# Optimization experiments

Measured on AMD Instinct MI355X. Metric: run time of the kernel, lower is better.

Reference implementation:

```python
import jax, jax.numpy as jnp
from jax import lax
import numpy as np

T = 8   # num_samples
D = 7   # num_nodes
K = 3   # topk


def _normalize(v):
    return v / jnp.maximum(jnp.linalg.norm(v, axis=-1, keepdims=True), 1e-12)


def _pool(x):
    # AdaptiveMaxPool2d(1): [B,H,N,C,h,w] -> [B,H,N,C]
    return x.max(axis=(-2, -1))


def _sepconv(x, dw, dwb, pw, pwb):
    # depthwise 3x3 (pad 1) + pointwise 1x1, NCHW
    c = x.shape[1]
    y = lax.conv_general_dilated(x, dw, (1, 1), ((1, 1), (1, 1)),
                                 dimension_numbers=('NCHW', 'OIHW', 'NCHW'),
                                 feature_group_count=c)
    y = y + dwb[None, :, None, None]
    y = lax.conv_general_dilated(y, pw, (1, 1), 'VALID',
                                 dimension_numbers=('NCHW', 'OIHW', 'NCHW'))
    return y + pwb[None, :, None, None]


def _conv_iter(x, A, dw, dwb, pw, pwb):
    # x: [B,H,N,C,h,w], A: [B,H,M,N] -> aggregate then sepconv update
    x = jnp.einsum('bhnm,bhmcij->bhncij', A, x)
    B, H, N, C, h, w = x.shape
    y = x.transpose(0, 2, 1, 3, 4, 5).reshape(B * N, H * C, h, w)
    y = _sepconv(y, dw, dwb, pw, pwb)
    return y.reshape(B, N, H, C, h, w).transpose(0, 2, 1, 3, 4, 5)


def reference(x, alpha_if, alpha_tm1, alpha_rev, alpha_tm2,
              bias_if, bias_tm1, bias_rev, bias_tm2,
              if_dw, if_dwb, if_pw, if_pwb,
              tm1_dw, tm1_dwb, tm1_pw, tm1_pwb,
              rev_dw, rev_dwb, rev_pw, rev_pwb,
              tm2_dw, tm2_dwb, tm2_pw, tm2_pwb,
              tr_dw, tr_dwb, tr_pw, tr_pwb):
    B, H, Nall, C, hh, ww = x.shape
    normal = x[:, :, 1:]            # [B,H,T*D,C,h,w]
    master = x[:, :, 0:1]           # [B,H,1,C,h,w]
    # 'b h (t d) c i j -> (b t) h d c i j'
    normal = normal.reshape(B, H, T, D, C, hh, ww).transpose(0, 2, 1, 3, 4, 5, 6).reshape(B * T, H, D, C, hh, ww)

    # inter-frame adjacency
    vn = _normalize(_pool(normal))
    A = jax.nn.softmax(jnp.einsum('bhnc,bhmc->bhnm', vn, vn) / alpha_if + bias_if, axis=-1)
    normal = _conv_iter(normal, A, if_dw, if_dwb, if_pw, if_pwb)

    # to master 1
    temp = normal.reshape(B, T, H, D, C, hh, ww).transpose(0, 2, 1, 3, 4, 5, 6).reshape(B, H, T * D, C, hh, ww)
    all_node = jnp.concatenate([master, temp], axis=2)   # [B,H,57,...]
    vn = _normalize(_pool(all_node))
    A = jax.nn.softmax(jnp.einsum('bhnc,bhmc->bhnm', vn[:, :, 0:1], vn) / alpha_tm1 + bias_tm1, axis=-1)
    master = _conv_iter(all_node, A, tm1_dw, tm1_dwb, tm1_pw, tm1_pwb)  # [B,H,1,C,h,w]

    # transform normal nodes
    Bt = B * T
    y = normal.transpose(0, 2, 1, 3, 4, 5).reshape(Bt * D, H * C, hh, ww)
    y = _sepconv(y, tr_dw, tr_dwb, tr_pw, tr_pwb)
    normal = y.reshape(Bt, D, H, C, hh, ww).transpose(0, 2, 1, 3, 4, 5)

    # reverse: topk MOST-DISSIMILAR frames (largest=False on similarity)
    temp = normal.reshape(B, T, H, D, C, hh, ww).transpose(0, 2, 1, 3, 4, 5, 6)  # [B,H,T,D,C,h,w]
    main = temp[:, :, :, -1]                                 # [B,H,T,C,h,w]
    mv = _normalize(_pool(main))                              # [B,H,T,C]
    Asim = jnp.einsum('bhtc,bhsc->bhts', mv, mv)
    idx = lax.top_k(-Asim, K)[1]                              # [B,H,T,K] smallest-sim frames
    bi = jnp.arange(B)[:, None, None, None]
    hi = jnp.arange(H)[None, :, None, None]
    sel = temp[bi, hi, idx]                                   # [B,H,T,K,D,C,h,w]
    different = sel.transpose(0, 2, 1, 3, 4, 5, 6, 7).reshape(Bt, H, K * D, C, hh, ww)

    vd = _normalize(_pool(different))
    vo = _normalize(_pool(normal))
    A = jax.nn.softmax(-jnp.einsum('bhnc,bhmc->bhnm', vo, vd) / alpha_rev + bias_rev, axis=-1)
    normal = _conv_iter(different, A, rev_dw, rev_dwb, rev_pw, rev_pwb) + normal

    # to master 2
    temp = normal.reshape(B, T, H, D, C, hh, ww).transpose(0, 2, 1, 3, 4, 5, 6).reshape(B, H, T * D, C, hh, ww)
    all_node = jnp.concatenate([master, temp], axis=2)
    vn = _normalize(_pool(all_node))
    A = jax.nn.softmax(jnp.einsum('bhnc,bhmc->bhnm', vn[:, :, 0:1], vn) / alpha_tm2 + bias_tm2, axis=-1)
    master = _conv_iter(all_node, A, tm2_dw, tm2_dwb, tm2_pw, tm2_pwb)
    return master[:, :, 0]                                    # [B,H,C,h,w]


def setup_inputs() -> dict:
    key = jax.random.key(0)
    ks = jax.random.split(key, 16)
    B, H, C, hh, ww = 4, 4, 128, 14, 14
    DIM = 512
    w_scale = 0.05

    def sep(k):
        k1, k2 = jax.random.split(k)
        return (jax.random.normal(k1, (DIM, 1, 3, 3), jnp.float32) * w_scale,
                jnp.zeros((DIM,), jnp.float32),
                jax.random.normal(k2, (DIM, DIM, 1, 1), jnp.float32) * w_scale,
                jnp.zeros((DIM,), jnp.float32))

    if_dw, if_dwb, if_pw, if_pwb = sep(ks[1])
    tm1_dw, tm1_dwb, tm1_pw, tm1_pwb = sep(ks[2])
    rev_dw, rev_dwb, rev_pw, rev_pwb = sep(ks[3])
    tm2_dw, tm2_dwb, tm2_pw, tm2_pwb = sep(ks[4])
    tr_dw, tr_dwb, tr_pw, tr_pwb = sep(ks[5])

    return dict(
        x=jax.random.normal(ks[0], (B, H, 1 + T * D, C, hh, ww), jnp.float32),
        alpha_if=jnp.ones((), jnp.float32), alpha_tm1=jnp.ones((), jnp.float32),
        alpha_rev=jnp.ones((), jnp.float32), alpha_tm2=jnp.ones((), jnp.float32),
        bias_if=jnp.zeros((D, D), jnp.float32),
        bias_tm1=jnp.zeros((1, 1 + T * D), jnp.float32),
        bias_rev=jnp.zeros((D, K * D), jnp.float32),
        bias_tm2=jnp.zeros((1, 1 + T * D), jnp.float32),
        if_dw=if_dw, if_dwb=if_dwb, if_pw=if_pw, if_pwb=if_pwb,
        tm1_dw=tm1_dw, tm1_dwb=tm1_dwb, tm1_pw=tm1_pw, tm1_pwb=tm1_pwb,
        rev_dw=rev_dw, rev_dwb=rev_dwb, rev_pw=rev_pw, rev_pwb=rev_pwb,
        tm2_dw=tm2_dw, tm2_dwb=tm2_dwb, tm2_pw=tm2_pw, tm2_pwb=tm2_pwb,
        tr_dw=tr_dw, tr_dwb=tr_dwb, tr_pw=tr_pw, tr_pwb=tr_pwb,
    )
```

## Files before the change

### kernel.cpp

```cpp
#include <hip/hip_runtime.h>
#include <hip/hip_bf16.h>
#include <float.h>
#include <math.h>

#define B_    4
#define H_    4
#define T_    8
#define D_    7
#define C_    128
#define HH_   14
#define S_    196
#define S4_   49
#define BT_   32
#define HC_   512
#define NODE_ 57
#define K_    3
#define KD_   21

#define BIG_  (BT_*D_*HC_*S_)
#define MS_   (B_*HC_*S_)
#define UB_   (BT_*D_*S_)
#define UM_   (B_*S_)
#define UMP_  896
#define NT_   24
#define WS_   1024

typedef unsigned short u16;
typedef unsigned int   u32;
typedef short bf16x8 __attribute__((ext_vector_type(8)));
typedef float f32x4  __attribute__((ext_vector_type(4)));

__device__ __forceinline__ float wave_max(float v){
    #pragma unroll
    for(int o=32;o>0;o>>=1) v = fmaxf(v, __shfl_xor(v,o,64));
    return v;
}
__device__ __forceinline__ float wave_sum(float v){
    #pragma unroll
    for(int o=32;o>0;o>>=1) v += __shfl_xor(v,o,64);
    return v;
}
__device__ __forceinline__ u16 f2bf(float f){
    u32 u = __float_as_uint(f);
    u += 0x7FFF + ((u>>16)&1);
    return (u16)(u>>16);
}
__device__ __forceinline__ float bf2f(u16 h){ return __uint_as_float(((u32)h)<<16); }

__device__ __forceinline__ void gld16(const void* g, void* l){
    __builtin_amdgcn_global_load_lds(
        (__attribute__((address_space(1))) void*)(void*)g,
        (__attribute__((address_space(3))) void*)l, 16, 0, 0);
}

__global__ void k_pool_x(const float* __restrict__ x, float* __restrict__ out){
    int v = blockIdx.x*4 + (threadIdx.x>>6);
    int lane = threadIdx.x & 63;
    int c = v & (C_-1);
    int r = v >> 7;
    int d = r % D_; r /= D_;
    int h = r & (H_-1); r >>= 2;
    int bt = r;
    int b = bt >> 3, t = bt & 7;
    const float* row = x + ((size_t)((b*H_+h)*NODE_ + 1 + t*D_ + d)*C_ + c)*S_;
    float m = -FLT_MAX;
    for(int s=lane; s<S_; s+=64) m = fmaxf(m, row[s]);
    m = wave_max(m);
    if(lane==0) out[v] = m;
}

__global__ void k_pool_conv(const float* __restrict__ in, float* __restrict__ out){
    int v = blockIdx.x*4 + (threadIdx.x>>6);
    int lane = threadIdx.x & 63;
    int c = v & (C_-1);
    int r = v >> 7;
    int d = r % D_; r /= D_;
    int h = r & (H_-1); r >>= 2;
    int bt = r;
    const float* row = in + ((size_t)((bt*D_+d)*HC_ + h*C_ + c))*S_;
    float m = -FLT_MAX;
    for(int s=lane; s<S_; s+=64) m = fmaxf(m, row[s]);
    m = wave_max(m);
    if(lane==0) out[v] = m;
}

__global__ void k_pool_x_master(const float* __restrict__ x, float* __restrict__ out){
    int v = blockIdx.x*4 + (threadIdx.x>>6);
    int lane = threadIdx.x & 63;
    int c = v & (C_-1);
    int h = (v>>7) & (H_-1);
    int b = v >> 9;
    const float* row = x + ((size_t)((b*H_+h)*NODE_)*C_ + c)*S_;
    float m = -FLT_MAX;
    for(int s=lane; s<S_; s+=64) m = fmaxf(m, row[s]);
    m = wave_max(m);
    if(lane==0) out[v] = m;
}

__global__ void k_pool_m1(const float* __restrict__ in, float* __restrict__ out){
    int v = blockIdx.x*4 + (threadIdx.x>>6);
    int lane = threadIdx.x & 63;
    int c = v & (C_-1);
    int h = (v>>7) & (H_-1);
    int b = v >> 9;
    const float* row = in + ((size_t)(b*HC_ + h*C_ + c))*S_;
    float m = -FLT_MAX;
    for(int s=lane; s<S_; s+=64) m = fmaxf(m, row[s]);
    m = wave_max(m);
    if(lane==0) out[v] = m;
}

__global__ void k_normalize(float* __restrict__ v){
    int vec = blockIdx.x;
    float val = v[(size_t)vec*C_ + threadIdx.x];
    float ss = wave_sum(val*val);
    __shared__ float sh[2];
    if((threadIdx.x&63)==0) sh[threadIdx.x>>6] = ss;
    __syncthreads();
    float tot = sh[0]+sh[1];
    v[(size_t)vec*C_ + threadIdx.x] = val / fmaxf(sqrtf(tot), 1e-12f);
}

__global__ void k_A_if(const float* __restrict__ vn, const float* __restrict__ bias,
                       const float* __restrict__ alpha_p, float* __restrict__ A){
    int bh = blockIdx.x;
    __shared__ float vs[D_*C_];
    __shared__ float z[D_][D_];
    for(int e=threadIdx.x; e<D_*C_; e+=64) vs[e] = vn[(size_t)bh*D_*C_ + e];
    __syncthreads();
    float alpha = alpha_p[0];
    if(threadIdx.x < D_*D_){
        int n = threadIdx.x/D_, m = threadIdx.x%D_;
        float acc=0.f;
        for(int c=0;c<C_;c++) acc += vs[n*C_+c]*vs[m*C_+c];
        z[n][m] = acc/alpha + bias[n*D_+m];
    }
    __syncthreads();
    if(threadIdx.x < D_){
        int n = threadIdx.x;
        float mx=-FLT_MAX;
        for(int m=0;m<D_;m++) mx=fmaxf(mx,z[n][m]);
        float e[D_]; float sum=0.f;
        for(int m=0;m<D_;m++){ e[m]=expf(z[n][m]-mx); sum+=e[m]; }
        for(int m=0;m<D_;m++) A[((size_t)bh*D_+n)*D_+m] = e[m]/sum;
    }
}

__global__ void k_A_tm(const float* __restrict__ vm, const float* __restrict__ vnrm,
                       const float* __restrict__ bias, const float* __restrict__ alpha_p,
                       float* __restrict__ A){
    int bh = blockIdx.x;
    int b = bh>>2, h = bh&3;
    __shared__ float v0[C_];
    __shared__ float z[NODE_];
    for(int e=threadIdx.x;e<C_;e+=64) v0[e]=vm[(size_t)bh*C_+e];
    __syncthreads();
    float alpha=alpha_p[0];
    if(threadIdx.x<NODE_){
        int m=threadIdx.x;
        float acc=0.f;
        if(m==0){
            for(int c=0;c<C_;c++) acc+=v0[c]*v0[c];
        } else {
            int t=(m-1)/D_, d=(m-1)%D_;
            const float* vp = vnrm + (size_t)(((b*T_+t)*H_+h)*D_+d)*C_;
            for(int c=0;c<C_;c++) acc+=v0[c]*vp[c];
        }
        z[m]=acc/alpha + bias[m];
    }
    __syncthreads();
    if(threadIdx.x==0){
        float mx=-FLT_MAX;
        for(int m=0;m<NODE_;m++) mx=fmaxf(mx,z[m]);
        float sum=0.f;
        for(int m=0;m<NODE_;m++){ z[m]=expf(z[m]-mx); sum+=z[m]; }
        for(int m=0;m<NODE_;m++) A[(size_t)bh*NODE_+m]=z[m]/sum;
    }
}

__global__ void k_topk(const float* __restrict__ voHat, int* __restrict__ idx){
    int bh = blockIdx.x;
    int b = bh>>2, h = bh&3;
    __shared__ float mv[T_][C_];
    __shared__ float As[T_][T_];
    for(int e=threadIdx.x;e<T_*C_;e+=64){
        int t=e>>7, c=e&(C_-1);
        mv[t][c]=voHat[(size_t)(((b*T_+t)*H_+h)*D_+(D_-1))*C_+c];
    }
    __syncthreads();
    {
        int t=threadIdx.x>>3, s2=threadIdx.x&7;
        float acc=0.f;
        for(int c=0;c<C_;c++) acc+=mv[t][c]*mv[s2][c];
        As[t][s2]=acc;
    }
    __syncthreads();
    if(threadIdx.x<T_){
        int t=threadIdx.x;
        bool used[T_];
        for(int j=0;j<T_;j++) used[j]=false;
        for(int k=0;k<K_;k++){
            float mn=FLT_MAX; int bi=0;
            for(int s2=0;s2<T_;s2++){
                if(!used[s2] && As[t][s2]<mn){ mn=As[t][s2]; bi=s2; }
            }
            used[bi]=true;
            idx[((size_t)bh*T_+t)*K_+k]=bi;
        }
    }
}

__global__ void k_A_rev(const float* __restrict__ voHat, const int* __restrict__ idx,
                        const float* __restrict__ bias, const float* __restrict__ alpha_p,
                        float* __restrict__ A){
    int bth = blockIdx.x;
    int bt = bth>>2, h = bth&3;
    int b = bt>>3, t = bt&7;
    __shared__ float vo[D_][C_];
    __shared__ float vd[KD_][C_];
    __shared__ float z[D_][KD_];
    for(int e=threadIdx.x;e<D_*C_;e+=256){
        int n=e>>7, c=e&(C_-1);
        vo[n][c]=voHat[(size_t)((bt*H_+h)*D_+n)*C_+c];
    }
    for(int e=threadIdx.x;e<KD_*C_;e+=256){
        int m=e>>7, c=e&(C_-1);
        int k=m/D_, dp=m%D_;
        int tt=idx[((size_t)(b*H_+h)*T_+t)*K_+k];
        vd[m][c]=voHat[(size_t)(((b*T_+tt)*H_+h)*D_+dp)*C_+c];
    }
    __syncthreads();
    float alpha=alpha_p[0];
    if(threadIdx.x<D_*KD_){
        int n=threadIdx.x/KD_, m=threadIdx.x%KD_;
        float acc=0.f;
        for(int c=0;c<C_;c++) acc+=vo[n][c]*vd[m][c];
        z[n][m] = -acc/alpha + bias[n*KD_+m];
    }
    __syncthreads();
    if(threadIdx.x<D_){
        int n=threadIdx.x;
        float mx=-FLT_MAX;
        for(int m=0;m<KD_;m++) mx=fmaxf(mx,z[n][m]);
        float sum=0.f;
        for(int m=0;m<KD_;m++){ z[n][m]=expf(z[n][m]-mx); sum+=z[n][m]; }
        for(int m=0;m<KD_;m++) A[(size_t)((bt*H_+h)*D_+n)*KD_+m]=z[n][m]/sum;
    }
}

__global__ void k_agg_tm(const float* __restrict__ mastersrc, int master_is_x,
                         const float* __restrict__ normal, const float* __restrict__ A,
                         float* __restrict__ out){
    int v = blockIdx.x*256 + threadIdx.x;
    int s4 = v % S4_;
    int r  = v / S4_;
    int hc = r & (HC_-1);
    int b  = r >> 9;
    int h = hc >> 7, c = hc & (C_-1);
    const float* Ap = A + (size_t)(b*H_+h)*NODE_;
    f32x4 m0;
    if(master_is_x) m0 = *(const f32x4*)(mastersrc + ((size_t)((b*H_+h)*NODE_)*C_ + c)*S_ + s4*4);
    else            m0 = *(const f32x4*)(mastersrc + (size_t)(b*HC_+hc)*S_ + s4*4);
    f32x4 acc = Ap[0]*m0;
    for(int t=0;t<T_;t++){
        const float* np = normal + ((size_t)((b*T_+t)*D_)*HC_+hc)*S_ + s4*4;
        #pragma unroll
        for(int d=0;d<D_;d++)
            acc += Ap[1+t*D_+d] * *(const f32x4*)(np + (size_t)d*HC_*S_);
    }
    *(f32x4*)(out + (size_t)r*S_ + s4*4) = acc;
}

__device__ __forceinline__ void dw_split_tail(float (*ti)[S_], float (*to)[S_],
                                              const float* __restrict__ w,
                                              const float* __restrict__ bias,
                                              int img, int ch0,
                                              u16* __restrict__ Xh, u16* __restrict__ Xl){
    int tid = threadIdx.x;
    for(int e=tid; e<16*S_; e+=256){
        int chl = e/S_, s = e - (e/S_)*S_;
        int ch = ch0 + chl;
        int y = s/HH_, xx = s - (s/HH_)*HH_;
        float acc = bias[ch];
        #pragma unroll
        for(int ky=0;ky<3;ky++){
            int yy=y+ky-1;
            if(yy<0||yy>=HH_) continue;
            #pragma unroll
            for(int kx=0;kx<3;kx++){
                int xx2=xx+kx-1;
                if(xx2<0||xx2>=HH_) continue;
                acc += ti[chl][yy*HH_+xx2]*w[ch*9+ky*3+kx];
            }
        }
        to[chl][s]=acc;
    }
    __syncthreads();
    for(int e=tid; e<16*S_; e+=256){
        int s = e>>4, chl = e&15;
        float f = to[chl][s];
        u16 h = f2bf(f);
        float lo = f - bf2f(h);
        size_t o = ((size_t)img*S_ + s)*HC_ + ch0 + chl;
        Xh[o] = h;
        Xl[o] = f2bf(lo);
    }
}

__launch_bounds__(256)
__global__ void k_dwsplit(const float* __restrict__ in, const float* __restrict__ w,
                          const float* __restrict__ bias,
                          u16* __restrict__ Xh, u16* __restrict__ Xl){
    int img = blockIdx.x >> 5;
    int ch0 = (blockIdx.x & 31) * 16;
    __shared__ float ti[16][S_];
    __shared__ float to[16][S_];
    int tid = threadIdx.x;
    for(int e=tid; e<16*S4_; e+=256){
        int chl = e/S4_, s4 = e - (e/S4_)*S4_;
        *(f32x4*)&ti[chl][s4*4] =
            *(const f32x4*)(in + ((size_t)img*HC_ + ch0 + chl)*S_ + s4*4);
    }
    __syncthreads();
    dw_split_tail(ti, to, w, bias, img, ch0, Xh, Xl);
}

__launch_bounds__(256)
__global__ void k_dwsplit_pool(const float* __restrict__ in, const float* __restrict__ w,
                               const float* __restrict__ bias,
                               u16* __restrict__ Xh, u16* __restrict__ Xl,
                               float* __restrict__ pooled){
    int img = blockIdx.x >> 5;
    int ch0 = (blockIdx.x & 31) * 16;
    __shared__ float ti[16][S_];
    __shared__ float to[16][S_];
    __shared__ float pm[16][17];
    int tid = threadIdx.x;
    for(int e=tid; e<16*S4_; e+=256){
        int chl = e/S4_, s4 = e - (e/S4_)*S4_;
        *(f32x4*)&ti[chl][s4*4] =
            *(const f32x4*)(in + ((size_t)img*HC_ + ch0 + chl)*S_ + s4*4);
    }
    __syncthreads();
    dw_split_tail(ti, to, w, bias, img, ch0, Xh, Xl);
    {
        int chl = tid & 15, g = tid >> 4;
        float m = -FLT_MAX;
        for(int s=g; s<S_; s+=16) m = fmaxf(m, ti[chl][s]);
        pm[chl][g] = m;
    }
    __syncthreads();
    if(tid < 16){
        float mm = -FLT_MAX;
        #pragma unroll
        for(int g2=0; g2<16; g2++) mm = fmaxf(mm, pm[tid][g2]);
        int bt = img/7, d = img - (img/7)*7;
        pooled[(size_t)((bt*4 + (ch0>>7))*7 + d)*C_ + (ch0 & 127) + tid] = mm;
    }
}

__launch_bounds__(256)
__global__ void k_fused_if(const float* __restrict__ x, const float* __restrict__ A,
                           const float* __restrict__ w, const float* __restrict__ bias,
                           u16* __restrict__ Xh, u16* __restrict__ Xl){
    int img = blockIdx.x >> 5;
    int ch0 = (blockIdx.x & 31) * 16;
    int bt = img/7, d = img - bt*7;
    int b = bt >> 3, t = bt & 7;
    int h = ch0 >> 7, c0 = ch0 & 127;
    __shared__ float ti[16][S_];
    __shared__ float to[16][S_];
    float a[D_];
    #pragma unroll
    for(int m=0;m<D_;m++) a[m] = A[(size_t)((bt*4+h)*D_ + d)*D_ + m];
    int tid = threadIdx.x;
    const float* xb = x + ((size_t)((b*H_+h)*NODE_ + 1 + t*D_)*C_ + c0)*S_;
    for(int e=tid; e<16*S4_; e+=256){
        int chl = e/S4_, s4 = e - (e/S4_)*S4_;
        const f32x4* xp = (const f32x4*)(xb + (size_t)chl*S_) + s4;
        f32x4 acc = {0.f,0.f,0.f,0.f};
        #pragma unroll
        for(int m=0;m<D_;m++) acc += a[m]*xp[(size_t)m*C_*S4_];
        *(f32x4*)&ti[chl][s4*4] = acc;
    }
    __syncthreads();
    dw_split_tail(ti, to, w, bias, img, ch0, Xh, Xl);
}

__launch_bounds__(256)
__global__ void k_fused_rev(const float* __restrict__ n2, const float* __restrict__ A,
                            const int* __restrict__ idx,
                            const float* __restrict__ w, const float* __restrict__ bias,
                            u16* __restrict__ Xh, u16* __restrict__ Xl){
    int img = blockIdx.x >> 5;
    int ch0 = (blockIdx.x & 31) * 16;
    int bt = img/7, d = img - bt*7;
    int b = bt >> 3, t = bt & 7;
    int h = ch0 >> 7;
    __shared__ float ti[16][S_];
    __shared__ float to[16][S_];
    float a[KD_];
    #pragma unroll
    for(int j=0;j<KD_;j++) a[j] = A[(size_t)((bt*4+h)*D_ + d)*KD_ + j];
    int tt0 = idx[((size_t)(b*H_+h)*T_+t)*K_+0];
    int tt1 = idx[((size_t)(b*H_+h)*T_+t)*K_+1];
    int tt2 = idx[((size_t)(b*H_+h)*T_+t)*K_+2];
    const f32x4* p0 = (const f32x4*)(n2 + ((size_t)((b*T_+tt0)*D_)*HC_ + ch0)*S_);
    const f32x4* p1 = (const f32x4*)(n2 + ((size_t)((b*T_+tt1)*D_)*HC_ + ch0)*S_);
    const f32x4* p2 = (const f32x4*)(n2 + ((size_t)((b*T_+tt2)*D_)*HC_ + ch0)*S_);
    int tid = threadIdx.x;
    for(int e=tid; e<16*S4_; e+=256){
        int chl = e/S4_, s4 = e - (e/S4_)*S4_;
        size_t off = (size_t)chl*S4_ + s4;
        f32x4 acc = {0.f,0.f,0.f,0.f};
        #pragma unroll
        for(int dp=0;dp<D_;dp++){
            size_t o2 = off + (size_t)dp*HC_*S4_;
            acc += a[dp]      * p0[o2];
            acc += a[D_+dp]   * p1[o2];
            acc += a[2*D_+dp] * p2[o2];
        }
        *(f32x4*)&ti[chl][s4*4] = acc;
    }
    __syncthreads();
    dw_split_tail(ti, to, w, bias, img, ch0, Xh, Xl);
}

__global__ void k_prepW(const float* __restrict__ Wg, u16* __restrict__ Waug){
    int i = blockIdx.x*256 + threadIdx.x;
    int oc = i >> 9, ic = i & 511;
    float f = Wg[i];
    u16 h = f2bf(f);
    float lo = f - bf2f(h);
    size_t base = (size_t)oc*WS_;
    Waug[base + ic]       = h;
    Waug[base + 512 + ic] = f2bf(lo);
}

__launch_bounds__(512)
__global__ void k_pwmfma(const u16* __restrict__ Xh, const u16* __restrict__ Xl,
                         const u16* __restrict__ Waug, const float* __restrict__ bias,
                         const float* __restrict__ res, float* __restrict__ out,
                         int nwg, int utot){
    __shared__ u16 SM[2][16384];
    const int tid  = threadIdx.x;
    const int q = nwg >> 3, r = nwg & 7;
    int xcd = blockIdx.x & 7, j = blockIdx.x >> 3;
    int L = xcd*q + (xcd < r ? xcd : r) + j;
    const int u0   = (L >> 2) * 128;
    const int oc0  = (L & 3) * 128;
    const int lane = tid & 63;
    const int w    = tid >> 6;
    const int wr   = w >> 1, wc = w & 1;
    const int l15  = lane & 15, lg = lane >> 4;

    f32x4 acc[2][4];
    #pragma unroll
    for(int mi=0;mi<2;mi++)
        #pragma unroll
        for(int ni=0;ni<4;ni++)
            acc[mi][ni] = (f32x4){0.f,0.f,0.f,0.f};

    auto STAGE = [&](int t){
        int jj, wk, xk; const u16* Xp;
        if(t < 16){ jj = t>>1; wk = (t&1) ? 512 + jj*64 : jj*64; Xp = Xh; xk = jj*64; }
        else      { jj = t-16; wk = jj*64;                        Xp = Xl; xk = jj*64; }
        u16* Asb = SM[t&1];
        u16* Bsb = Asb + 8192;
        #pragma unroll
        for(int i=0;i<2;i++){
            int seg = w*2 + i;
            int row = seg*8 + (lane>>3);
            int cg  = (lane&7) ^ (lane>>3);
            gld16(Waug + (size_t)(oc0+row)*WS_ + wk + cg*8, Asb + seg*512);
            gld16(Xp   + (size_t)(u0 +row)*512 + xk + cg*8, Bsb + seg*512);
        }
    };
    auto COMPUTE = [&](int cur){
        const u16* Asb = SM[cur];
        const u16* Bsb = SM[cur] + 8192;
        #pragma unroll
        for(int ks=0;ks<2;ks++){
            bf16x8 a[2], b[4];
            #pragma unroll
            for(int mi=0;mi<2;mi++){
                int row = wr*32 + mi*16 + l15;
                int ch  = ((ks<<2) + lg) ^ (row & 7);
                a[mi] = *(const bf16x8*)(Asb + row*64 + ch*8);
            }
            #pragma unroll
            for(int ni=0;ni<4;ni++){
                int row = wc*64 + ni*16 + l15;
                int ch  = ((ks<<2) + lg) ^ (row & 7);
                b[ni] = *(const bf16x8*)(Bsb + row*64 + ch*8);
            }
            #pragma unroll
            for(int mi=0;mi<2;mi++)
                #pragma unroll
                for(int ni=0;ni<4;ni++)
                    acc[mi][ni] = __builtin_amdgcn_mfma_f32_16x16x32_bf16(a[mi], b[ni], acc[mi][ni], 0,0,0);
        }
    };

    STAGE(0);
    for(int t=0; t<NT_; t++){
        if(t+1 < NT_){
            STAGE(t+1);
            asm volatile("s_waitcnt vmcnt(4)" ::: "memory");
        } else {
            asm volatile("s_waitcnt vmcnt(0)" ::: "memory");
        }
        __builtin_amdgcn_s_barrier();
        asm volatile("" ::: "memory");
        COMPUTE(t&1);
        asm volatile("" ::: "memory");
        __builtin_amdgcn_s_barrier();
    }

    #pragma unroll
    for(int ni=0;ni<4;ni++){
        int u = u0 + wc*64 + ni*16 + l15;
        if(u >= utot) continue;
        int img = u / S_, s = u - img*S_;
        #pragma unroll
        for(int mi=0;mi<2;mi++){
            int ocb = oc0 + wr*32 + mi*16 + lg*4;
            #pragma unroll
            for(int q2=0;q2<4;q2++){
                int oc = ocb + q2;
                size_t oidx = ((size_t)img*HC_ + oc)*S_ + s;
                float v = acc[mi][ni][q2] + bias[oc];
                if(res) v += res[oidx];
                out[oidx] = v;
            }
        }
    }
}

extern "C" void kernel_launch(void* const* d_in, const int* in_sizes, int n_in,
                              void* d_out, int out_size, void* d_ws, size_t ws_size,
                              hipStream_t stream){
    (void)in_sizes; (void)n_in; (void)out_size; (void)ws_size;
    const float* x         = (const float*)d_in[0];
    const float* alpha_if  = (const float*)d_in[1];
    const float* alpha_tm1 = (const float*)d_in[2];
    const float* alpha_rev = (const float*)d_in[3];
    const float* alpha_tm2 = (const float*)d_in[4];
    const float* bias_if   = (const float*)d_in[5];
    const float* bias_tm1  = (const float*)d_in[6];
    const float* bias_rev  = (const float*)d_in[7];
    const float* bias_tm2  = (const float*)d_in[8];
    const float* if_dw =(const float*)d_in[9];  const float* if_dwb =(const float*)d_in[10];
    const float* if_pw =(const float*)d_in[11]; const float* if_pwb =(const float*)d_in[12];
    const float* tm1_dw=(const float*)d_in[13]; const float* tm1_dwb=(const float*)d_in[14];
    const float* tm1_pw=(const float*)d_in[15]; const float* tm1_pwb=(const float*)d_in[16];
    const float* rev_dw=(const float*)d_in[17]; const float* rev_dwb=(const float*)d_in[18];
    const float* rev_pw=(const float*)d_in[19]; const float* rev_pwb=(const float*)d_in[20];
    const float* tm2_dw=(const float*)d_in[21]; const float* tm2_dwb=(const float*)d_in[22];
    const float* tm2_pw=(const float*)d_in[23]; const float* tm2_pwb=(const float*)d_in[24];
    const float* tr_dw =(const float*)d_in[25]; const float* tr_dwb =(const float*)d_in[26];
    const float* tr_pw =(const float*)d_in[27]; const float* tr_pwb =(const float*)d_in[28];

    float* ws = (float*)d_ws;
    float* G0      = ws;
    float* G1      = G0 + (size_t)BIG_;
    u16*   Xh      = (u16*)(ws + 2*(size_t)BIG_);
    u16*   Xl      = Xh + (size_t)BIG_;
    u16*   WA0     = Xl + (size_t)BIG_;
    u16*   WA1     = WA0 + 512*WS_;
    u16*   WA2     = WA1 + 512*WS_;
    u16*   WA3     = WA2 + 512*WS_;
    u16*   WA4     = WA3 + 512*WS_;
    u16*   XhM     = WA4 + 512*WS_;
    u16*   XlM     = XhM + (size_t)UMP_*HC_;
    float* master1 = (float*)(XlM + (size_t)UMP_*HC_);
    float* Ma      = master1 + MS_;
    float* pooledN = Ma + MS_;
    float* pooledM = pooledN + BT_*H_*D_*C_;
    float* Aif     = pooledM + B_*H_*C_;
    float* Atm1    = Aif + BT_*H_*D_*D_;
    float* Arev    = Atm1 + B_*H_*NODE_;
    float* Atm2    = Arev + BT_*H_*D_*KD_;
    int*   idxb    = (int*)(Atm2 + B_*H_*NODE_);
    float* out     = (float*)d_out;

    const int NV  = BT_*H_*D_*C_;
    const int gemmGrid  = (UB_/128)*4;
    const int gemmGridM = (UMP_/128)*4;
    const int dsGrid  = BT_*D_*32;
    const int dsGridM = B_*32;
    float* null_res = nullptr;

    k_prepW<<<1024, 256, 0, stream>>>(if_pw,  WA0);
    k_prepW<<<1024, 256, 0, stream>>>(tr_pw,  WA1);
    k_prepW<<<1024, 256, 0, stream>>>(rev_pw, WA2);
    k_prepW<<<1024, 256, 0, stream>>>(tm1_pw, WA3);
    k_prepW<<<1024, 256, 0, stream>>>(tm2_pw, WA4);

    k_pool_x   <<<NV/4, 256, 0, stream>>>(x, pooledN);
    k_normalize<<<NV/C_, 128, 0, stream>>>(pooledN);
    k_A_if     <<<BT_*H_, 64, 0, stream>>>(pooledN, bias_if, alpha_if, Aif);
    k_fused_if <<<dsGrid, 256, 0, stream>>>(x, Aif, if_dw, if_dwb, Xh, Xl);
    k_pwmfma   <<<gemmGrid, 512, 0, stream>>>(Xh, Xl, WA0, if_pwb, null_res, G1, gemmGrid, UB_);

    k_dwsplit_pool<<<dsGrid, 256, 0, stream>>>(G1, tr_dw, tr_dwb, Xh, Xl, pooledN);
    k_normalize<<<NV/C_, 128, 0, stream>>>(pooledN);
    k_pool_x_master<<<(B_*H_*C_)/4, 256, 0, stream>>>(x, pooledM);
    k_normalize<<<B_*H_, 128, 0, stream>>>(pooledM);
    k_A_tm     <<<B_*H_, 64, 0, stream>>>(pooledM, pooledN, bias_tm1, alpha_tm1, Atm1);
    k_agg_tm   <<<MS_/1024, 256, 0, stream>>>(x, 1, G1, Atm1, Ma);
    k_dwsplit  <<<dsGridM, 256, 0, stream>>>(Ma, tm1_dw, tm1_dwb, XhM, XlM);
    k_pwmfma   <<<gemmGridM, 512, 0, stream>>>(XhM, XlM, WA3, tm1_pwb, null_res, master1, gemmGridM, UM_);
    k_pwmfma   <<<gemmGrid, 512, 0, stream>>>(Xh, Xl, WA1, tr_pwb, null_res, G0, gemmGrid, UB_);

    k_pool_conv<<<NV/4, 256, 0, stream>>>(G0, pooledN);
    k_normalize<<<NV/C_, 128, 0, stream>>>(pooledN);
    k_topk     <<<B_*H_, 64, 0, stream>>>(pooledN, idxb);
    k_A_rev    <<<BT_*H_, 256, 0, stream>>>(pooledN, idxb, bias_rev, alpha_rev, Arev);
    k_fused_rev<<<dsGrid, 256, 0, stream>>>(G0, Arev, idxb, rev_dw, rev_dwb, Xh, Xl);
    k_pwmfma   <<<gemmGrid, 512, 0, stream>>>(Xh, Xl, WA2, rev_pwb, G0, G1, gemmGrid, UB_);

    k_pool_conv<<<NV/4, 256, 0, stream>>>(G1, pooledN);
    k_normalize<<<NV/C_, 128, 0, stream>>>(pooledN);
    k_pool_m1  <<<(B_*H_*C_)/4, 256, 0, stream>>>(master1, pooledM);
    k_normalize<<<B_*H_, 128, 0, stream>>>(pooledM);
    k_A_tm     <<<B_*H_, 64, 0, stream>>>(pooledM, pooledN, bias_tm2, alpha_tm2, Atm2);
    k_agg_tm   <<<MS_/1024, 256, 0, stream>>>(master1, 0, G1, Atm2, Ma);
    k_dwsplit  <<<dsGridM, 256, 0, stream>>>(Ma, tm2_dw, tm2_dwb, XhM, XlM);
    k_pwmfma   <<<gemmGridM, 512, 0, stream>>>(XhM, XlM, WA4, tm2_pwb, null_res, out, gemmGridM, UM_);
}
```

Measured before the change: 933.6 us.

## Stage source node tiles in shared memory and reuse across all output nodes

The fused aggregation+depthwise kernels now assign each block a (bt, 4-channel) slice and load all source nodes into LDS once, then loop over the 7 destination nodes, computing the aggregation, depthwise conv and bf16 split for each. This removes the redundant global reads where each destination node previously re-read all D (or 3·D) source nodes. In exchange, the grid becomes smaller (4096 blocks), only 196 of 256 threads do the aggregation, the loop over d adds syncs, and the rev variant uses about 66KB of LDS, which limits occupancy. Output writes shrink to 4-channel (8-byte) stores.

```diff
diff --git a/kernel.cpp b/kernel.cpp
--- a/kernel.cpp
+++ b/kernel.cpp
@@ -29,6 +29,7 @@
 typedef unsigned int   u32;
 typedef short bf16x8 __attribute__((ext_vector_type(8)));
 typedef float f32x4  __attribute__((ext_vector_type(4)));
+typedef unsigned short u16x4 __attribute__((ext_vector_type(4)));
 
 __device__ __forceinline__ float wave_max(float v){
     #pragma unroll
@@ -359,32 +360,77 @@
     }
 }
 
+__device__ __forceinline__ void dw_split_tail4(const float* __restrict__ ti, float* __restrict__ to,
+                                               const float* __restrict__ w,
+                                               const float* __restrict__ bias,
+                                               int img, int ch0,
+                                               u16* __restrict__ Xh, u16* __restrict__ Xl){
+    int tid = threadIdx.x;
+    for(int e=tid; e<4*S_; e+=256){
+        int chl = e/S_, s = e - (e/S_)*S_;
+        int ch = ch0 + chl;
+        int y = s/HH_, xx = s - (s/HH_)*HH_;
+        float acc = bias[ch];
+        #pragma unroll
+        for(int ky=0;ky<3;ky++){
+            int yy=y+ky-1;
+            if(yy<0||yy>=HH_) continue;
+            #pragma unroll
+            for(int kx=0;kx<3;kx++){
+                int xx2=xx+kx-1;
+                if(xx2<0||xx2>=HH_) continue;
+                acc += ti[chl*S_ + yy*HH_+xx2]*w[ch*9+ky*3+kx];
+            }
+        }
+        to[e]=acc;
+    }
+    __syncthreads();
+    if(tid < S_){
+        int s = tid;
+        u16x4 hv, lv;
+        #pragma unroll
+        for(int chl=0;chl<4;chl++){
+            float f = to[chl*S_ + s];
+            u16 hh = f2bf(f);
+            hv[chl] = hh;
+            lv[chl] = f2bf(f - bf2f(hh));
+        }
+        size_t o = ((size_t)img*S_ + s)*HC_ + ch0;
+        *(u16x4*)(Xh + o) = hv;
+        *(u16x4*)(Xl + o) = lv;
+    }
+}
+
 __launch_bounds__(256)
 __global__ void k_fused_if(const float* __restrict__ x, const float* __restrict__ A,
                            const float* __restrict__ w, const float* __restrict__ bias,
                            u16* __restrict__ Xh, u16* __restrict__ Xl){
-    int img = blockIdx.x >> 5;
-    int ch0 = (blockIdx.x & 31) * 16;
-    int bt = img/7, d = img - bt*7;
+    int bt  = blockIdx.x >> 7;
+    int ch0 = (blockIdx.x & 127) * 4;
+    int h = ch0 >> 7;
     int b = bt >> 3, t = bt & 7;
-    int h = ch0 >> 7, c0 = ch0 & 127;
-    __shared__ float ti[16][S_];
-    __shared__ float to[16][S_];
-    float a[D_];
-    #pragma unroll
-    for(int m=0;m<D_;m++) a[m] = A[(size_t)((bt*4+h)*D_ + d)*D_ + m];
+    __shared__ float src[D_*4*S_];
+    __shared__ float ti[4*S_];
+    __shared__ float to[4*S_];
     int tid = threadIdx.x;
-    const float* xb = x + ((size_t)((b*H_+h)*NODE_ + 1 + t*D_)*C_ + c0)*S_;
-    for(int e=tid; e<16*S4_; e+=256){
-        int chl = e/S4_, s4 = e - (e/S4_)*S4_;
-        const f32x4* xp = (const f32x4*)(xb + (size_t)chl*S_) + s4;
-        f32x4 acc = {0.f,0.f,0.f,0.f};
-        #pragma unroll
-        for(int m=0;m<D_;m++) acc += a[m]*xp[(size_t)m*C_*S4_];
-        *(f32x4*)&ti[chl][s4*4] = acc;
-    }
-    __syncthreads();
-    dw_split_tail(ti, to, w, bias, img, ch0, Xh, Xl);
+    const float* xb = x + ((size_t)((b*H_+h)*NODE_ + 1 + t*D_)*C_ + (ch0 & 127))*S_;
+    for(int e=tid; e<D_*S_; e+=256){
+        int m = e/S_, v = e - (e/S_)*S_;
+        *(f32x4*)&src[m*4*S_ + v*4] = *(const f32x4*)(xb + (size_t)m*C_*S_ + v*4);
+    }
+    __syncthreads();
+    const float* Ab = A + (size_t)((bt*4+h)*D_)*D_;
+    for(int d=0; d<D_; d++){
+        if(tid < S_){
+            f32x4 acc = {0.f,0.f,0.f,0.f};
+            #pragma unroll
+            for(int m=0;m<D_;m++) acc += Ab[d*D_+m] * *(const f32x4*)&src[m*4*S_ + tid*4];
+            *(f32x4*)&ti[tid*4] = acc;
+        }
+        __syncthreads();
+        dw_split_tail4(ti, to, w, bias, bt*D_+d, ch0, Xh, Xl);
+        __syncthreads();
+    }
 }
 
 __launch_bounds__(256)
@@ -392,38 +438,39 @@
                             const int* __restrict__ idx,
                             const float* __restrict__ w, const float* __restrict__ bias,
                             u16* __restrict__ Xh, u16* __restrict__ Xl){
-    int img = blockIdx.x >> 5;
-    int ch0 = (blockIdx.x & 31) * 16;
-    int bt = img/7, d = img - bt*7;
+    int bt  = blockIdx.x >> 7;
+    int ch0 = (blockIdx.x & 127) * 4;
+    int h = ch0 >> 7;
     int b = bt >> 3, t = bt & 7;
-    int h = ch0 >> 7;
-    __shared__ float ti[16][S_];
-    __shared__ float to[16][S_];
-    float a[KD_];
-    #pragma unroll
-    for(int j=0;j<KD_;j++) a[j] = A[(size_t)((bt*4+h)*D_ + d)*KD_ + j];
+    __shared__ float src[KD_*4*S_];
+    __shared__ float ti[4*S_];
+    __shared__ float to[4*S_];
+    int tid = threadIdx.x;
     int tt0 = idx[((size_t)(b*H_+h)*T_+t)*K_+0];
     int tt1 = idx[((size_t)(b*H_+h)*T_+t)*K_+1];
     int tt2 = idx[((size_t)(b*H_+h)*T_+t)*K_+2];
-    const f32x4* p0 = (const f32x4*)(n2 + ((size_t)((b*T_+tt0)*D_)*HC_ + ch0)*S_);
-    const f32x4* p1 = (const f32x4*)(n2 + ((size_t)((b*T_+tt1)*D_)*HC_ + ch0)*S_);
-    const f32x4* p2 = (const f32x4*)(n2 + ((size_t)((b*T_+tt2)*D_)*HC_ + ch0)*S_);
-    int tid = threadIdx.x;
-    for(int e=tid; e<16*S4_; e+=256){
-        int chl = e/S4_, s4 = e - (e/S4_)*S4_;
-        size_t off = (size_t)chl*S4_ + s4;
-        f32x4 acc = {0.f,0.f,0.f,0.f};
-        #pragma unroll
-        for(int dp=0;dp<D_;dp++){
-            size_t o2 = off + (size_t)dp*HC_*S4_;
-            acc += a[dp]      * p0[o2];
-            acc += a[D_+dp]   * p1[o2];
-            acc += a[2*D_+dp] * p2[o2];
-        }
-        *(f32x4*)&ti[chl][s4*4] = acc;
-    }
-    __syncthreads();
-    dw_split_tail(ti, to, w, bias, img, ch0, Xh, Xl);
+    const float* base0 = n2 + ((size_t)((b*T_+tt0)*D_)*HC_ + ch0)*S_;
+    const float* base1 = n2 + ((size_t)((b*T_+tt1)*D_)*HC_ + ch0)*S_;
+    const float* base2 = n2 + ((size_t)((b*T_+tt2)*D_)*HC_ + ch0)*S_;
+    for(int e=tid; e<KD_*S_; e+=256){
+        int j = e/S_, v = e - (e/S_)*S_;
+        int k = j/D_, dp = j - k*D_;
+        const float* bk = (k==0) ? base0 : (k==1) ? base1 : base2;
+        *(f32x4*)&src[j*4*S_ + v*4] = *(const f32x4*)(bk + (size_t)dp*HC_*S_ + v*4);
+    }
+    __syncthreads();
+    const float* Ab = A + (size_t)((bt*4+h)*D_)*KD_;
+    for(int d=0; d<D_; d++){
+        if(tid < S_){
+            f32x4 acc = {0.f,0.f,0.f,0.f};
+            #pragma unroll
+            for(int j=0;j<KD_;j++) acc += Ab[d*KD_+j] * *(const f32x4*)&src[j*4*S_ + tid*4];
+            *(f32x4*)&ti[tid*4] = acc;
+        }
+        __syncthreads();
+        dw_split_tail4(ti, to, w, bias, bt*D_+d, ch0, Xh, Xl);
+        __syncthreads();
+    }
 }
 
 __global__ void k_prepW(const float* __restrict__ Wg, u16* __restrict__ Waug){
@@ -587,8 +634,9 @@
     const int NV  = BT_*H_*D_*C_;
     const int gemmGrid  = (UB_/128)*4;
     const int gemmGridM = (UMP_/128)*4;
-    const int dsGrid  = BT_*D_*32;
-    const int dsGridM = B_*32;
+    const int dsGrid    = BT_*D_*32;
+    const int dsGridM   = B_*32;
+    const int fusedGrid = BT_*128;
     float* null_res = nullptr;
 
     k_prepW<<<1024, 256, 0, stream>>>(if_pw,  WA0);
@@ -600,7 +648,7 @@
     k_pool_x   <<<NV/4, 256, 0, stream>>>(x, pooledN);
     k_normalize<<<NV/C_, 128, 0, stream>>>(pooledN);
     k_A_if     <<<BT_*H_, 64, 0, stream>>>(pooledN, bias_if, alpha_if, Aif);
-    k_fused_if <<<dsGrid, 256, 0, stream>>>(x, Aif, if_dw, if_dwb, Xh, Xl);
+    k_fused_if <<<fusedGrid, 256, 0, stream>>>(x, Aif, if_dw, if_dwb, Xh, Xl);
     k_pwmfma   <<<gemmGrid, 512, 0, stream>>>(Xh, Xl, WA0, if_pwb, null_res, G1, gemmGrid, UB_);
 
     k_dwsplit_pool<<<dsGrid, 256, 0, stream>>>(G1, tr_dw, tr_dwb, Xh, Xl, pooledN);
@@ -617,7 +665,7 @@
     k_normalize<<<NV/C_, 128, 0, stream>>>(pooledN);
     k_topk     <<<B_*H_, 64, 0, stream>>>(pooledN, idxb);
     k_A_rev    <<<BT_*H_, 256, 0, stream>>>(pooledN, idxb, bias_rev, alpha_rev, Arev);
-    k_fused_rev<<<dsGrid, 256, 0, stream>>>(G0, Arev, idxb, rev_dw, rev_dwb, Xh, Xl);
+    k_fused_rev<<<fusedGrid, 256, 0, stream>>>(G0, Arev, idxb, rev_dw, rev_dwb, Xh, Xl);
     k_pwmfma   <<<gemmGrid, 512, 0, stream>>>(Xh, Xl, WA2, rev_pwb, G0, G1, gemmGrid, UB_);
 
     k_pool_conv<<<NV/4, 256, 0, stream>>>(G1, pooledN);
```

Result: slower. 1.162 ms (+24.5%).

## Compute all seven output nodes per block to reuse loaded source tiles

Applied to the files above, without the earlier changes.

The inter-frame and reverse aggregation kernels now have each block handle all D output nodes for one (bt, channel-group) pair instead of one node. Each source node tile is loaded once and accumulated into seven register accumulators, so global reads of x and G0 drop about sevenfold. The cost is a grid seven times smaller (1024 blocks), heavy register use from 28 f32x4 accumulators per thread, and a serial loop of seven depthwise-split tails with extra barriers inside each block.

```diff
diff --git a/kernel.cpp b/kernel.cpp
--- a/kernel.cpp
+++ b/kernel.cpp
@@ -24,6 +24,7 @@
 #define UMP_  896
 #define NT_   24
 #define WS_   1024
+#define NE4_  784
 
 typedef unsigned short u16;
 typedef unsigned int   u32;
@@ -363,28 +364,50 @@
 __global__ void k_fused_if(const float* __restrict__ x, const float* __restrict__ A,
                            const float* __restrict__ w, const float* __restrict__ bias,
                            u16* __restrict__ Xh, u16* __restrict__ Xl){
-    int img = blockIdx.x >> 5;
+    int bt  = blockIdx.x >> 5;
     int ch0 = (blockIdx.x & 31) * 16;
-    int bt = img/7, d = img - bt*7;
+    int h = ch0 >> 7, c0 = ch0 & 127;
     int b = bt >> 3, t = bt & 7;
-    int h = ch0 >> 7, c0 = ch0 & 127;
+    __shared__ float Ash[D_*D_];
     __shared__ float ti[16][S_];
     __shared__ float to[16][S_];
-    float a[D_];
-    #pragma unroll
-    for(int m=0;m<D_;m++) a[m] = A[(size_t)((bt*4+h)*D_ + d)*D_ + m];
     int tid = threadIdx.x;
+    if(tid < D_*D_) Ash[tid] = A[(size_t)((bt*4+h)*D_)*D_ + tid];
+    __syncthreads();
     const float* xb = x + ((size_t)((b*H_+h)*NODE_ + 1 + t*D_)*C_ + c0)*S_;
-    for(int e=tid; e<16*S4_; e+=256){
-        int chl = e/S4_, s4 = e - (e/S4_)*S4_;
-        const f32x4* xp = (const f32x4*)(xb + (size_t)chl*S_) + s4;
-        f32x4 acc = {0.f,0.f,0.f,0.f};
-        #pragma unroll
-        for(int m=0;m<D_;m++) acc += a[m]*xp[(size_t)m*C_*S4_];
-        *(f32x4*)&ti[chl][s4*4] = acc;
-    }
-    __syncthreads();
-    dw_split_tail(ti, to, w, bias, img, ch0, Xh, Xl);
+    f32x4 acc[D_][4];
+    #pragma unroll
+    for(int d=0;d<D_;d++)
+        #pragma unroll
+        for(int q=0;q<4;q++) acc[d][q] = (f32x4){0.f,0.f,0.f,0.f};
+    #pragma unroll
+    for(int m=0;m<D_;m++){
+        const f32x4* sp = (const f32x4*)(xb + (size_t)m*C_*S_);
+        f32x4 v[4];
+        #pragma unroll
+        for(int q=0;q<4;q++){
+            int e4 = tid + q*256;
+            v[q] = (e4 < NE4_) ? sp[e4] : (f32x4){0.f,0.f,0.f,0.f};
+        }
+        #pragma unroll
+        for(int d=0;d<D_;d++){
+            float a = Ash[d*D_+m];
+            #pragma unroll
+            for(int q=0;q<4;q++) acc[d][q] += a*v[q];
+        }
+    }
+    float* tif = &ti[0][0];
+    #pragma unroll
+    for(int d=0;d<D_;d++){
+        __syncthreads();
+        #pragma unroll
+        for(int q=0;q<4;q++){
+            int e4 = tid + q*256;
+            if(e4 < NE4_) *(f32x4*)&tif[e4*4] = acc[d][q];
+        }
+        __syncthreads();
+        dw_split_tail(ti, to, w, bias, bt*D_+d, ch0, Xh, Xl);
+    }
 }
 
 __launch_bounds__(256)
@@ -392,38 +415,57 @@
                             const int* __restrict__ idx,
                             const float* __restrict__ w, const float* __restrict__ bias,
                             u16* __restrict__ Xh, u16* __restrict__ Xl){
-    int img = blockIdx.x >> 5;
+    int bt  = blockIdx.x >> 5;
     int ch0 = (blockIdx.x & 31) * 16;
-    int bt = img/7, d = img - bt*7;
+    int h = ch0 >> 7;
     int b = bt >> 3, t = bt & 7;
-    int h = ch0 >> 7;
+    __shared__ float Ash[D_*KD_];
+    __shared__ int tts[3];
     __shared__ float ti[16][S_];
     __shared__ float to[16][S_];
-    float a[KD_];
-    #pragma unroll
-    for(int j=0;j<KD_;j++) a[j] = A[(size_t)((bt*4+h)*D_ + d)*KD_ + j];
-    int tt0 = idx[((size_t)(b*H_+h)*T_+t)*K_+0];
-    int tt1 = idx[((size_t)(b*H_+h)*T_+t)*K_+1];
-    int tt2 = idx[((size_t)(b*H_+h)*T_+t)*K_+2];
-    const f32x4* p0 = (const f32x4*)(n2 + ((size_t)((b*T_+tt0)*D_)*HC_ + ch0)*S_);
-    const f32x4* p1 = (const f32x4*)(n2 + ((size_t)((b*T_+tt1)*D_)*HC_ + ch0)*S_);
-    const f32x4* p2 = (const f32x4*)(n2 + ((size_t)((b*T_+tt2)*D_)*HC_ + ch0)*S_);
     int tid = threadIdx.x;
-    for(int e=tid; e<16*S4_; e+=256){
-        int chl = e/S4_, s4 = e - (e/S4_)*S4_;
-        size_t off = (size_t)chl*S4_ + s4;
-        f32x4 acc = {0.f,0.f,0.f,0.f};
-        #pragma unroll
-        for(int dp=0;dp<D_;dp++){
-            size_t o2 = off + (size_t)dp*HC_*S4_;
-            acc += a[dp]      * p0[o2];
-            acc += a[D_+dp]   * p1[o2];
-            acc += a[2*D_+dp] * p2[o2];
-        }
-        *(f32x4*)&ti[chl][s4*4] = acc;
-    }
-    __syncthreads();
-    dw_split_tail(ti, to, w, bias, img, ch0, Xh, Xl);
+    if(tid < D_*KD_) Ash[tid] = A[(size_t)((bt*4+h)*D_)*KD_ + tid];
+    if(tid>=160 && tid<163)
+        tts[tid-160] = idx[((size_t)(b*H_+h)*T_+t)*K_ + (tid-160)];
+    __syncthreads();
+    const float* bases[K_];
+    #pragma unroll
+    for(int k=0;k<K_;k++)
+        bases[k] = n2 + ((size_t)((b*T_+tts[k])*D_)*HC_ + ch0)*S_;
+    f32x4 acc[D_][4];
+    #pragma unroll
+    for(int d=0;d<D_;d++)
+        #pragma unroll
+        for(int q=0;q<4;q++) acc[d][q] = (f32x4){0.f,0.f,0.f,0.f};
+    #pragma unroll
+    for(int j=0;j<KD_;j++){
+        const int k = j/D_, dp = j - (j/D_)*D_;
+        const f32x4* sp = (const f32x4*)(bases[k] + (size_t)dp*HC_*S_);
+        f32x4 v[4];
+        #pragma unroll
+        for(int q=0;q<4;q++){
+            int e4 = tid + q*256;
+            v[q] = (e4 < NE4_) ? sp[e4] : (f32x4){0.f,0.f,0.f,0.f};
+        }
+        #pragma unroll
+        for(int d=0;d<D_;d++){
+            float a = Ash[d*KD_+j];
+            #pragma unroll
+            for(int q=0;q<4;q++) acc[d][q] += a*v[q];
+        }
+    }
+    float* tif = &ti[0][0];
+    #pragma unroll
+    for(int d=0;d<D_;d++){
+        __syncthreads();
+        #pragma unroll
+        for(int q=0;q<4;q++){
+            int e4 = tid + q*256;
+            if(e4 < NE4_) *(f32x4*)&tif[e4*4] = acc[d][q];
+        }
+        __syncthreads();
+        dw_split_tail(ti, to, w, bias, bt*D_+d, ch0, Xh, Xl);
+    }
 }
 
 __global__ void k_prepW(const float* __restrict__ Wg, u16* __restrict__ Waug){
@@ -587,8 +629,9 @@
     const int NV  = BT_*H_*D_*C_;
     const int gemmGrid  = (UB_/128)*4;
     const int gemmGridM = (UMP_/128)*4;
-    const int dsGrid  = BT_*D_*32;
-    const int dsGridM = B_*32;
+    const int dsGrid    = BT_*D_*32;
+    const int dsGridM   = B_*32;
+    const int fusedGrid = BT_*32;
     float* null_res = nullptr;
 
     k_prepW<<<1024, 256, 0, stream>>>(if_pw,  WA0);
@@ -600,7 +643,7 @@
     k_pool_x   <<<NV/4, 256, 0, stream>>>(x, pooledN);
     k_normalize<<<NV/C_, 128, 0, stream>>>(pooledN);
     k_A_if     <<<BT_*H_, 64, 0, stream>>>(pooledN, bias_if, alpha_if, Aif);
-    k_fused_if <<<dsGrid, 256, 0, stream>>>(x, Aif, if_dw, if_dwb, Xh, Xl);
+    k_fused_if <<<fusedGrid, 256, 0, stream>>>(x, Aif, if_dw, if_dwb, Xh, Xl);
     k_pwmfma   <<<gemmGrid, 512, 0, stream>>>(Xh, Xl, WA0, if_pwb, null_res, G1, gemmGrid, UB_);
 
     k_dwsplit_pool<<<dsGrid, 256, 0, stream>>>(G1, tr_dw, tr_dwb, Xh, Xl, pooledN);
@@ -617,7 +660,7 @@
     k_normalize<<<NV/C_, 128, 0, stream>>>(pooledN);
     k_topk     <<<B_*H_, 64, 0, stream>>>(pooledN, idxb);
     k_A_rev    <<<BT_*H_, 256, 0, stream>>>(pooledN, idxb, bias_rev, alpha_rev, Arev);
-    k_fused_rev<<<dsGrid, 256, 0, stream>>>(G0, Arev, idxb, rev_dw, rev_dwb, Xh, Xl);
+    k_fused_rev<<<fusedGrid, 256, 0, stream>>>(G0, Arev, idxb, rev_dw, rev_dwb, Xh, Xl);
     k_pwmfma   <<<gemmGrid, 512, 0, stream>>>(Xh, Xl, WA2, rev_pwb, G0, G1, gemmGrid, UB_);
 
     k_pool_conv<<<NV/4, 256, 0, stream>>>(G1, pooledN);
```

Measured after the change: 1.390 ms. 48.8% more time.

## Fuse max-pooling into pointwise GEMM epilogue via order-preserving atomicMax keys

Applied to the files above, without the earlier changes.

Removes the two standalone k_pool_conv passes that re-read the full G0/G1 activations. Instead, the GEMM epilogue reduces per-tile channel maxima in LDS with atomicMax on sign-flipped integer keys, then issues global atomicMax. A new kernel decodes the keys and normalizes. This adds memsets, LDS and global atomics, and an extra barrier in the GEMM. Separately, dwsplit_pool now runs its pooling before the depthwise tail.

```diff
diff --git a/kernel.cpp b/kernel.cpp
--- a/kernel.cpp
+++ b/kernel.cpp
@@ -51,6 +51,11 @@
     __builtin_amdgcn_global_load_lds(
         (__attribute__((address_space(1))) void*)(void*)g,
         (__attribute__((address_space(3))) void*)l, 16, 0, 0);
+}
+
+__device__ __forceinline__ u32 fkey(float f){
+    u32 u = __float_as_uint(f);
+    return (u & 0x80000000u) ? ~u : (u | 0x80000000u);
 }
 
 __global__ void k_pool_x(const float* __restrict__ x, float* __restrict__ out){
@@ -69,21 +74,6 @@
     if(lane==0) out[v] = m;
 }
 
-__global__ void k_pool_conv(const float* __restrict__ in, float* __restrict__ out){
-    int v = blockIdx.x*4 + (threadIdx.x>>6);
-    int lane = threadIdx.x & 63;
-    int c = v & (C_-1);
-    int r = v >> 7;
-    int d = r % D_; r /= D_;
-    int h = r & (H_-1); r >>= 2;
-    int bt = r;
-    const float* row = in + ((size_t)((bt*D_+d)*HC_ + h*C_ + c))*S_;
-    float m = -FLT_MAX;
-    for(int s=lane; s<S_; s+=64) m = fmaxf(m, row[s]);
-    m = wave_max(m);
-    if(lane==0) out[v] = m;
-}
-
 __global__ void k_pool_x_master(const float* __restrict__ x, float* __restrict__ out){
     int v = blockIdx.x*4 + (threadIdx.x>>6);
     int lane = threadIdx.x & 63;
@@ -113,6 +103,19 @@
 __global__ void k_normalize(float* __restrict__ v){
     int vec = blockIdx.x;
     float val = v[(size_t)vec*C_ + threadIdx.x];
+    float ss = wave_sum(val*val);
+    __shared__ float sh[2];
+    if((threadIdx.x&63)==0) sh[threadIdx.x>>6] = ss;
+    __syncthreads();
+    float tot = sh[0]+sh[1];
+    v[(size_t)vec*C_ + threadIdx.x] = val / fmaxf(sqrtf(tot), 1e-12f);
+}
+
+__global__ void k_decode_normalize(float* __restrict__ v){
+    int vec = blockIdx.x;
+    u32 key = ((const u32*)v)[(size_t)vec*C_ + threadIdx.x];
+    u32 uu = (key & 0x80000000u) ? (key ^ 0x80000000u) : ~key;
+    float val = __uint_as_float(uu);
     float ss = wave_sum(val*val);
     __shared__ float sh[2];
     if((threadIdx.x&63)==0) sh[threadIdx.x>>6] = ss;
@@ -342,7 +345,6 @@
             *(const f32x4*)(in + ((size_t)img*HC_ + ch0 + chl)*S_ + s4*4);
     }
     __syncthreads();
-    dw_split_tail(ti, to, w, bias, img, ch0, Xh, Xl);
     {
         int chl = tid & 15, g = tid >> 4;
         float m = -FLT_MAX;
@@ -357,6 +359,8 @@
         int bt = img/7, d = img - (img/7)*7;
         pooled[(size_t)((bt*4 + (ch0>>7))*7 + d)*C_ + (ch0 & 127) + tid] = mm;
     }
+    __syncthreads();
+    dw_split_tail(ti, to, w, bias, img, ch0, Xh, Xl);
 }
 
 __launch_bounds__(256)
@@ -441,7 +445,7 @@
 __global__ void k_pwmfma(const u16* __restrict__ Xh, const u16* __restrict__ Xl,
                          const u16* __restrict__ Waug, const float* __restrict__ bias,
                          const float* __restrict__ res, float* __restrict__ out,
-                         int nwg, int utot){
+                         int nwg, int utot, u32* __restrict__ pooled){
     __shared__ u16 SM[2][16384];
     const int tid  = threadIdx.x;
     const int q = nwg >> 3, r = nwg & 7;
@@ -517,21 +521,45 @@
         __builtin_amdgcn_s_barrier();
     }
 
+    u32* pl = (u32*)&SM[0][0];
+    const int img0 = u0 / S_;
+    if(pooled){
+        if(tid < 256) pl[tid] = 0u;
+        __syncthreads();
+    }
+
     #pragma unroll
     for(int ni=0;ni<4;ni++){
         int u = u0 + wc*64 + ni*16 + l15;
         if(u >= utot) continue;
         int img = u / S_, s = u - img*S_;
+        int li = (img - img0) << 7;
         #pragma unroll
         for(int mi=0;mi<2;mi++){
-            int ocb = oc0 + wr*32 + mi*16 + lg*4;
+            int ocl = wr*32 + mi*16 + lg*4;
             #pragma unroll
             for(int q2=0;q2<4;q2++){
-                int oc = ocb + q2;
+                int oc = oc0 + ocl + q2;
                 size_t oidx = ((size_t)img*HC_ + oc)*S_ + s;
                 float v = acc[mi][ni][q2] + bias[oc];
                 if(res) v += res[oidx];
                 out[oidx] = v;
+                if(pooled) atomicMax(&pl[li + ocl + q2], fkey(v));
+            }
+        }
+    }
+
+    if(pooled){
+        __syncthreads();
+        if(tid < 256){
+            int li2 = tid >> 7, ocl = tid & 127;
+            int img = img0 + li2;
+            int ulast = (u0 + 127 < utot) ? (u0 + 127) : (utot - 1);
+            if(img <= ulast / S_){
+                int oc = oc0 + ocl;
+                int bt = img / D_, d = img - (img/D_)*D_;
+                int h = oc >> 7, c = oc & 127;
+                atomicMax(pooled + ((size_t)((bt*4+h)*D_ + d)*C_ + c), pl[tid]);
             }
         }
     }
@@ -587,9 +615,10 @@
     const int NV  = BT_*H_*D_*C_;
     const int gemmGrid  = (UB_/128)*4;
     const int gemmGridM = (UMP_/128)*4;
-    const int dsGrid  = BT_*D_*32;
-    const int dsGridM = B_*32;
+    const int dsGrid    = BT_*D_*32;
+    const int dsGridM   = B_*32;
     float* null_res = nullptr;
+    u32*   no_pool  = nullptr;
 
     k_prepW<<<1024, 256, 0, stream>>>(if_pw,  WA0);
     k_prepW<<<1024, 256, 0, stream>>>(tr_pw,  WA1);
@@ -601,7 +630,7 @@
     k_normalize<<<NV/C_, 128, 0, stream>>>(pooledN);
     k_A_if     <<<BT_*H_, 64, 0, stream>>>(pooledN, bias_if, alpha_if, Aif);
     k_fused_if <<<dsGrid, 256, 0, stream>>>(x, Aif, if_dw, if_dwb, Xh, Xl);
-    k_pwmfma   <<<gemmGrid, 512, 0, stream>>>(Xh, Xl, WA0, if_pwb, null_res, G1, gemmGrid, UB_);
+    k_pwmfma   <<<gemmGrid, 512, 0, stream>>>(Xh, Xl, WA0, if_pwb, null_res, G1, gemmGrid, UB_, no_pool);
 
     k_dwsplit_pool<<<dsGrid, 256, 0, stream>>>(G1, tr_dw, tr_dwb, Xh, Xl, pooledN);
     k_normalize<<<NV/C_, 128, 0, stream>>>(pooledN);
@@ -610,22 +639,22 @@
     k_A_tm     <<<B_*H_, 64, 0, stream>>>(pooledM, pooledN, bias_tm1, alpha_tm1, Atm1);
     k_agg_tm   <<<MS_/1024, 256, 0, stream>>>(x, 1, G1, Atm1, Ma);
     k_dwsplit  <<<dsGridM, 256, 0, stream>>>(Ma, tm1_dw, tm1_dwb, XhM, XlM);
-    k_pwmfma   <<<gemmGridM, 512, 0, stream>>>(XhM, XlM, WA3, tm1_pwb, null_res, master1, gemmGridM, UM_);
-    k_pwmfma   <<<gemmGrid, 512, 0, stream>>>(Xh, Xl, WA1, tr_pwb, null_res, G0, gemmGrid, UB_);
-
-    k_pool_conv<<<NV/4, 256, 0, stream>>>(G0, pooledN);
-    k_normalize<<<NV/C_, 128, 0, stream>>>(pooledN);
+    k_pwmfma   <<<gemmGridM, 512, 0, stream>>>(XhM, XlM, WA3, tm1_pwb, null_res, master1, gemmGridM, UM_, no_pool);
+    hipMemsetAsync(pooledN, 0, (size_t)NV*sizeof(float), stream);
+    k_pwmfma   <<<gemmGrid, 512, 0, stream>>>(Xh, Xl, WA1, tr_pwb, null_res, G0, gemmGrid, UB_, (u32*)pooledN);
+
+    k_decode_normalize<<<NV/C_, 128, 0, stream>>>(pooledN);
     k_topk     <<<B_*H_, 64, 0, stream>>>(pooledN, idxb);
     k_A_rev    <<<BT_*H_, 256, 0, stream>>>(pooledN, idxb, bias_rev, alpha_rev, Arev);
     k_fused_rev<<<dsGrid, 256, 0, stream>>>(G0, Arev, idxb, rev_dw, rev_dwb, Xh, Xl);
-    k_pwmfma   <<<gemmGrid, 512, 0, stream>>>(Xh, Xl, WA2, rev_pwb, G0, G1, gemmGrid, UB_);
-
-    k_pool_conv<<<NV/4, 256, 0, stream>>>(G1, pooledN);
-    k_normalize<<<NV/C_, 128, 0, stream>>>(pooledN);
+    hipMemsetAsync(pooledN, 0, (size_t)NV*sizeof(float), stream);
+    k_pwmfma   <<<gemmGrid, 512, 0, stream>>>(Xh, Xl, WA2, rev_pwb, G0, G1, gemmGrid, UB_, (u32*)pooledN);
+
+    k_decode_normalize<<<NV/C_, 128, 0, stream>>>(pooledN);
     k_pool_m1  <<<(B_*H_*C_)/4, 256, 0, stream>>>(master1, pooledM);
     k_normalize<<<B_*H_, 128, 0, stream>>>(pooledM);
     k_A_tm     <<<B_*H_, 64, 0, stream>>>(pooledM, pooledN, bias_tm2, alpha_tm2, Atm2);
     k_agg_tm   <<<MS_/1024, 256, 0, stream>>>(master1, 0, G1, Atm2, Ma);
     k_dwsplit  <<<dsGridM, 256, 0, stream>>>(Ma, tm2_dw, tm2_dwb, XhM, XlM);
-    k_pwmfma   <<<gemmGridM, 512, 0, stream>>>(XhM, XlM, WA4, tm2_pwb, null_res, out, gemmGridM, UM_);
-}
+    k_pwmfma   <<<gemmGridM, 512, 0, stream>>>(XhM, XlM, WA4, tm2_pwb, null_res, out, gemmGridM, UM_, no_pool);
+}
```

Result: slower. 965.5 us (+3.4%).
